# Performance work log

Hardware: AMD Instinct MI355X
Metric: run time of the kernel (lower is better)

## Reference

```python
import jax, jax.numpy as jnp
import numpy as np

N_NODES = 100000
N_EDGES = 800000
D_IN, D_H1, D_H2, D_OUT = 512, 256, 256, 64


def setup_inputs() -> dict:
    key = jax.random.key(0)
    ks = jax.random.split(key, 8)
    x = jax.random.normal(ks[0], (N_NODES, D_IN), dtype=jnp.float32)
    edge_index = jax.random.randint(ks[1], (2, N_EDGES), 0, N_NODES, dtype=jnp.int64)
    # Glorot-style scaled weights (PyG GCNConv uses glorot init; Linear uses kaiming-uniform).
    W1 = jax.random.normal(ks[2], (D_IN, D_H1), dtype=jnp.float32) / np.sqrt(D_IN)
    b1 = jnp.zeros((D_H1,), dtype=jnp.float32)
    W2 = jax.random.normal(ks[3], (D_H1, D_H2), dtype=jnp.float32) / np.sqrt(D_H1)
    b2 = jnp.zeros((D_H2,), dtype=jnp.float32)
    Wc = jax.random.normal(ks[4], (D_H2, D_OUT), dtype=jnp.float32) / np.sqrt(D_H2)
    bc = jnp.zeros((D_OUT,), dtype=jnp.float32)
    return {"x": x, "edge_index": edge_index, "W1": W1, "b1": b1,
            "W2": W2, "b2": b2, "Wc": Wc, "bc": bc}


def reference(x, edge_index, W1, b1, W2, b2, Wc, bc):
    # GCNModel.forward in eval mode (dropout is identity when training=False).
    N = x.shape[0]
    src, dst = edge_index[0], edge_index[1]
    # PyG GCNConv: add self-loops, symmetric normalization D^-1/2 (A+I) D^-1/2.
    deg = jnp.zeros((N,), x.dtype).at[dst].add(jnp.float32(1.0)) + 1.0  # in-degree + self-loop
    dinv = jax.lax.rsqrt(deg)                         # [N]
    norm = dinv[src] * dinv[dst]                      # [E] per-edge coefficient
    self_norm = (dinv * dinv)[:, None]                # [N,1] self-loop coefficient 1/deg

    def gcn_conv(h, W, b):
        h = h @ W                                     # transform first (PyG order)
        agg = jax.ops.segment_sum(h[src] * norm[:, None], dst, num_segments=N)
        return agg + h * self_norm + b

    h = jax.nn.relu(gcn_conv(x, W1, b1))
    h = jax.nn.relu(gcn_conv(h, W2, b2))
    return h @ Wc + bc                                # [N, num_classes]
```

## Files before the change

### kernel.cpp

```cpp
#include <hip/hip_runtime.h>
#include <cstdint>

#define DIN 512
#define DH  256
#define DOUT 64

typedef __attribute__((ext_vector_type(8))) short bf16x8;
typedef __attribute__((ext_vector_type(4))) float f32x4;
typedef unsigned int uint32;

__device__ __forceinline__ unsigned short f2bf(float f) {
    uint32 u = __float_as_uint(f);
    u += 0x7fff + ((u >> 16) & 1);
    return (unsigned short)(u >> 16);
}
__device__ __forceinline__ float bf2f(unsigned short h) {
    return __uint_as_float(((uint32)h) << 16);
}
__device__ __forceinline__ float bflo(uint32 u) { return __uint_as_float(u << 16); }
__device__ __forceinline__ float bfhi(uint32 u) { return __uint_as_float(u & 0xffff0000u); }
__device__ __forceinline__ uint32 pk2(float lo, float hi) {
    return (uint32)f2bf(lo) | ((uint32)f2bf(hi) << 16);
}

__global__ void detect_i64(const unsigned long long* ei, int n_check,
                           unsigned long long bound, int* flag) {
    __shared__ int ok;
    if (threadIdx.x == 0) ok = 1;
    __syncthreads();
    int bad = 0;
    for (int i = threadIdx.x; i < n_check; i += blockDim.x) {
        if (ei[i] >= bound) bad = 1;
    }
    if (bad) ok = 0;
    __syncthreads();
    if (threadIdx.x == 0) *flag = ok;
}

__device__ __forceinline__ int get_idx(const void* ei, int is64, int pos) {
    if (is64) return (int)((const long long*)ei)[pos];
    return ((const int*)ei)[pos];
}

__global__ void count_deg(const void* ei, const int* flag, int E, int* counts) {
    const int is64 = *flag;
    int e = blockIdx.x * blockDim.x + threadIdx.x;
    if (e >= E) return;
    int d = get_idx(ei, is64, E + e);
    atomicAdd(&counts[d], 1);
}

__global__ void compute_dinv(const int* counts, float* dinv, int N) {
    int i = blockIdx.x * blockDim.x + threadIdx.x;
    if (i < N) dinv[i] = rsqrtf((float)counts[i] + 1.0f);
}

#define SCAN_BLOCK 256
#define SCAN_ELEMS 1024

__global__ void scan1(const int* counts, int* out, int* blocksums, int N) {
    __shared__ int sh[SCAN_BLOCK];
    int base = blockIdx.x * SCAN_ELEMS;
    int t = threadIdx.x;
    int v[4];
    int s = 0;
    #pragma unroll
    for (int j = 0; j < 4; j++) {
        int idx = base + t * 4 + j;
        v[j] = (idx < N) ? counts[idx] : 0;
        s += v[j];
    }
    sh[t] = s;
    __syncthreads();
    for (int off = 1; off < SCAN_BLOCK; off <<= 1) {
        int x = (t >= off) ? sh[t - off] : 0;
        __syncthreads();
        sh[t] += x;
        __syncthreads();
    }
    int run = (t == 0) ? 0 : sh[t - 1];
    #pragma unroll
    for (int j = 0; j < 4; j++) {
        int idx = base + t * 4 + j;
        if (idx < N) out[idx] = run;
        run += v[j];
    }
    if (t == SCAN_BLOCK - 1) blocksums[blockIdx.x] = sh[t];
}

__global__ void scan2(int* blocksums, int NB) {
    __shared__ int sh[SCAN_BLOCK];
    int t = threadIdx.x;
    sh[t] = (t < NB) ? blocksums[t] : 0;
    __syncthreads();
    for (int off = 1; off < SCAN_BLOCK; off <<= 1) {
        int x = (t >= off) ? sh[t - off] : 0;
        __syncthreads();
        sh[t] += x;
        __syncthreads();
    }
    if (t < NB) blocksums[t] = (t == 0) ? 0 : sh[t - 1];
}

__global__ void scan3(int* row_ptr, const int* blocksums, int N, int E) {
    int i = blockIdx.x * blockDim.x + threadIdx.x;
    if (i < N) row_ptr[i] += blocksums[i / SCAN_ELEMS];
    if (i == N) row_ptr[N] = E;
}

__global__ void fill_csr(const void* ei, const int* flag, int E,
                         const int* row_ptr, int* cursor, int* col_idx,
                         const float* dinv, float* edge_w) {
    const int is64 = *flag;
    int e = blockIdx.x * blockDim.x + threadIdx.x;
    if (e >= E) return;
    int d = get_idx(ei, is64, E + e);
    int s = get_idx(ei, is64, e);
    int pos = row_ptr[d] + atomicAdd(&cursor[d], 1);
    col_idx[pos] = s;
    edge_w[pos] = dinv[s] * dinv[d];
}

__global__ void transpose_w(const float* __restrict__ W, unsigned short* __restrict__ Bt,
                            int K, int Nw) {
    int i = blockIdx.x * blockDim.x + threadIdx.x;
    if (i >= K * Nw) return;
    int k = i / Nw, n = i % Nw;
    Bt[(size_t)n * K + k] = f2bf(W[i]);
}

template <bool A_FP32>
__global__ __launch_bounds__(256) void gemm_mfma(const void* __restrict__ Ap,
                                                 const unsigned short* __restrict__ Bt,
                                                 unsigned short* __restrict__ C,
                                                 int M, int K) {
    __shared__ unsigned short lds[20480];
    unsigned short* As = lds;
    unsigned short* Bs = lds + 4096;
    const int tid = threadIdx.x;
    const int w = tid >> 6, l = tid & 63;
    const int m0 = blockIdx.x * 64;

    f32x4 acc[4][4] = {};

    for (int k0 = 0; k0 < K; k0 += 64) {
        #pragma unroll
        for (int i = 0; i < 8; i++) {
            int row = i * 32 + (tid >> 3);
            int gq = (tid & 7) ^ (row & 7);
            const unsigned short* src = Bt + (size_t)row * K + k0 + gq * 8;
            unsigned short* dst = Bs + row * 64 + (tid & 7) * 8;
            __builtin_amdgcn_global_load_lds(
                (const __attribute__((address_space(1))) uint32*)src,
                (__attribute__((address_space(3))) uint32*)dst, 16, 0, 0);
        }
        if (A_FP32) {
            const float* Af = (const float*)Ap;
            #pragma unroll
            for (int i = 0; i < 2; i++) {
                int row = i * 32 + (tid >> 3);
                int g = tid & 7;
                int rg = m0 + row; if (rg > M - 1) rg = M - 1;
                const float* s = Af + (size_t)rg * K + k0 + g * 8;
                float4 v0 = *(const float4*)s;
                float4 v1 = *(const float4*)(s + 4);
                uint4 o;
                o.x = pk2(v0.x, v0.y); o.y = pk2(v0.z, v0.w);
                o.z = pk2(v1.x, v1.y); o.w = pk2(v1.z, v1.w);
                *(uint4*)(As + row * 64 + ((g ^ (row & 7)) * 8)) = o;
            }
        } else {
            const unsigned short* Ab = (const unsigned short*)Ap;
            #pragma unroll
            for (int i = 0; i < 2; i++) {
                int row = i * 32 + (tid >> 3);
                int gq = (tid & 7) ^ (row & 7);
                int rg = m0 + row; if (rg > M - 1) rg = M - 1;
                const unsigned short* src = Ab + (size_t)rg * K + k0 + gq * 8;
                unsigned short* dst = As + row * 64 + (tid & 7) * 8;
                __builtin_amdgcn_global_load_lds(
                    (const __attribute__((address_space(1))) uint32*)src,
                    (__attribute__((address_space(3))) uint32*)dst, 16, 0, 0);
            }
        }
        __syncthreads();
        #pragma unroll
        for (int ks = 0; ks < 2; ks++) {
            bf16x8 a[4], b[4];
            #pragma unroll
            for (int m = 0; m < 4; m++) {
                int arow = m * 16 + (l & 15);
                int ag = (ks * 4 + (l >> 4)) ^ (arow & 7);
                a[m] = *(const bf16x8*)(As + arow * 64 + ag * 8);
            }
            #pragma unroll
            for (int n = 0; n < 4; n++) {
                int brow = w * 64 + n * 16 + (l & 15);
                int bg = (ks * 4 + (l >> 4)) ^ (brow & 7);
                b[n] = *(const bf16x8*)(Bs + brow * 64 + bg * 8);
            }
            #pragma unroll
            for (int m = 0; m < 4; m++)
                #pragma unroll
                for (int n = 0; n < 4; n++)
                    acc[m][n] = __builtin_amdgcn_mfma_f32_16x16x32_bf16(a[m], b[n], acc[m][n], 0, 0, 0);
        }
        __syncthreads();
    }

    unsigned short* ep = lds + w * 4096;
    #pragma unroll
    for (int m = 0; m < 4; m++)
        #pragma unroll
        for (int n = 0; n < 4; n++)
            #pragma unroll
            for (int r = 0; r < 4; r++)
                ep[(m * 16 + (l >> 4) * 4 + r) * 64 + n * 16 + (l & 15)] = f2bf(acc[m][n][r]);
    __syncthreads();
    #pragma unroll
    for (int p = 0; p < 8; p++) {
        int row = p * 8 + (l >> 3);
        int gr = m0 + row;
        uint4 v = *(const uint4*)(ep + row * 64 + (l & 7) * 8);
        if (gr < M)
            *(uint4*)(C + (size_t)gr * 256 + w * 64 + (l & 7) * 8) = v;
    }
}

__global__ __launch_bounds__(256) void gemm_head(const unsigned short* __restrict__ A,
                                                 const unsigned short* __restrict__ Bt,
                                                 const float* __restrict__ bias,
                                                 float* __restrict__ out, int M) {
    __shared__ unsigned short As[128 * 64];
    __shared__ unsigned short Bs[64 * 64];
    const int tid = threadIdx.x;
    const int w = tid >> 6, l = tid & 63;
    const int m0 = blockIdx.x * 128;
    const int wr = w >> 1, wc = w & 1;
    f32x4 acc[4][2] = {};

    for (int k0 = 0; k0 < 256; k0 += 64) {
        #pragma unroll
        for (int i = 0; i < 4; i++) {
            int row = i * 32 + (tid >> 3);
            int gq = (tid & 7) ^ (row & 7);
            int rg = m0 + row; if (rg > M - 1) rg = M - 1;
            __builtin_amdgcn_global_load_lds(
                (const __attribute__((address_space(1))) uint32*)(A + (size_t)rg * 256 + k0 + gq * 8),
                (__attribute__((address_space(3))) uint32*)(As + row * 64 + (tid & 7) * 8), 16, 0, 0);
        }
        #pragma unroll
        for (int i = 0; i < 2; i++) {
            int row = i * 32 + (tid >> 3);
            int gq = (tid & 7) ^ (row & 7);
            __builtin_amdgcn_global_load_lds(
                (const __attribute__((address_space(1))) uint32*)(Bt + (size_t)row * 256 + k0 + gq * 8),
                (__attribute__((address_space(3))) uint32*)(Bs + row * 64 + (tid & 7) * 8), 16, 0, 0);
        }
        __syncthreads();
        #pragma unroll
        for (int ks = 0; ks < 2; ks++) {
            bf16x8 a[4], b[2];
            #pragma unroll
            for (int m = 0; m < 4; m++) {
                int arow = wr * 64 + m * 16 + (l & 15);
                int ag = (ks * 4 + (l >> 4)) ^ (arow & 7);
                a[m] = *(const bf16x8*)(As + arow * 64 + ag * 8);
            }
            #pragma unroll
            for (int n = 0; n < 2; n++) {
                int brow = wc * 32 + n * 16 + (l & 15);
                int bg = (ks * 4 + (l >> 4)) ^ (brow & 7);
                b[n] = *(const bf16x8*)(Bs + brow * 64 + bg * 8);
            }
            #pragma unroll
            for (int m = 0; m < 4; m++)
                #pragma unroll
                for (int n = 0; n < 2; n++)
                    acc[m][n] = __builtin_amdgcn_mfma_f32_16x16x32_bf16(a[m], b[n], acc[m][n], 0, 0, 0);
        }
        __syncthreads();
    }
    #pragma unroll
    for (int m = 0; m < 4; m++)
        #pragma unroll
        for (int n = 0; n < 2; n++)
            #pragma unroll
            for (int r = 0; r < 4; r++) {
                int gr = m0 + wr * 64 + m * 16 + (l >> 4) * 4 + r;
                int col = wc * 32 + n * 16 + (l & 15);
                if (gr < M) out[(size_t)gr * 64 + col] = acc[m][n][r] + bias[col];
            }
}

#define ACC8(v, wgt)                                    \
    do {                                                \
        acc[0] = fmaf(wgt, bflo(v.x), acc[0]);          \
        acc[1] = fmaf(wgt, bfhi(v.x), acc[1]);          \
        acc[2] = fmaf(wgt, bflo(v.y), acc[2]);          \
        acc[3] = fmaf(wgt, bfhi(v.y), acc[3]);          \
        acc[4] = fmaf(wgt, bflo(v.z), acc[4]);          \
        acc[5] = fmaf(wgt, bfhi(v.z), acc[5]);          \
        acc[6] = fmaf(wgt, bflo(v.w), acc[6]);          \
        acc[7] = fmaf(wgt, bfhi(v.w), acc[7]);          \
    } while (0)

__global__ __launch_bounds__(256) void aggregate_bf(const unsigned short* __restrict__ t,
                                                    const float* __restrict__ dinv,
                                                    const int* __restrict__ row_ptr,
                                                    const int* __restrict__ col_idx,
                                                    const float* __restrict__ edge_w,
                                                    const float* __restrict__ bias,
                                                    unsigned short* __restrict__ outb,
                                                    int N) {
    int wave = threadIdx.x >> 6;
    int lane = threadIdx.x & 63;
    int half = lane >> 5;
    int sl = lane & 31;
    int n = blockIdx.x * 8 + wave * 2 + half;
    if (n >= N) return;

    float dn = dinv[n];
    int r0 = row_ptr[n], r1 = row_ptr[n + 1];

    float acc[8];
    {
        uint4 sv = *(const uint4*)(t + (size_t)n * DH + sl * 8);
        float sn = dn * dn;
        acc[0] = bflo(sv.x) * sn; acc[1] = bfhi(sv.x) * sn;
        acc[2] = bflo(sv.y) * sn; acc[3] = bfhi(sv.y) * sn;
        acc[4] = bflo(sv.z) * sn; acc[5] = bfhi(sv.z) * sn;
        acc[6] = bflo(sv.w) * sn; acc[7] = bfhi(sv.w) * sn;
    }

    int j = r0;
    for (; j + 4 <= r1; j += 4) {
        int s0 = col_idx[j + 0], s1 = col_idx[j + 1];
        int s2 = col_idx[j + 2], s3 = col_idx[j + 3];
        float w0 = edge_w[j + 0], w1 = edge_w[j + 1];
        float w2 = edge_w[j + 2], w3 = edge_w[j + 3];
        uint4 v0 = *(const uint4*)(t + (size_t)s0 * DH + sl * 8);
        uint4 v1 = *(const uint4*)(t + (size_t)s1 * DH + sl * 8);
        uint4 v2 = *(const uint4*)(t + (size_t)s2 * DH + sl * 8);
        uint4 v3 = *(const uint4*)(t + (size_t)s3 * DH + sl * 8);
        ACC8(v0, w0); ACC8(v1, w1); ACC8(v2, w2); ACC8(v3, w3);
    }
    for (; j < r1; j++) {
        int s = col_idx[j];
        float wgt = edge_w[j];
        uint4 v = *(const uint4*)(t + (size_t)s * DH + sl * 8);
        ACC8(v, wgt);
    }

    float4 b0 = *(const float4*)(bias + sl * 8);
    float4 b1v = *(const float4*)(bias + sl * 8 + 4);
    acc[0] = fmaxf(acc[0] + b0.x, 0.f);  acc[1] = fmaxf(acc[1] + b0.y, 0.f);
    acc[2] = fmaxf(acc[2] + b0.z, 0.f);  acc[3] = fmaxf(acc[3] + b0.w, 0.f);
    acc[4] = fmaxf(acc[4] + b1v.x, 0.f); acc[5] = fmaxf(acc[5] + b1v.y, 0.f);
    acc[6] = fmaxf(acc[6] + b1v.z, 0.f); acc[7] = fmaxf(acc[7] + b1v.w, 0.f);

    uint4 o;
    o.x = pk2(acc[0], acc[1]);
    o.y = pk2(acc[2], acc[3]);
    o.z = pk2(acc[4], acc[5]);
    o.w = pk2(acc[6], acc[7]);
    *(uint4*)(outb + (size_t)n * DH + sl * 8) = o;
}

extern "C" void kernel_launch(void* const* d_in, const int* in_sizes, int n_in,
                              void* d_out, int out_size, void* d_ws, size_t ws_size,
                              hipStream_t stream) {
    const float* x  = (const float*)d_in[0];
    const void*  ei = d_in[1];
    const float* W1 = (const float*)d_in[2];
    const float* b1 = (const float*)d_in[3];
    const float* W2 = (const float*)d_in[4];
    const float* b2 = (const float*)d_in[5];
    const float* Wc = (const float*)d_in[6];
    const float* bc = (const float*)d_in[7];
    float* out = (float*)d_out;

    const int N = in_sizes[0] / DIN;
    const int E = in_sizes[1] / 2;

    char* ws = (char*)d_ws;
    size_t off = 0;
    auto alloc = [&](size_t bytes) -> void* {
        off = (off + 255) & ~(size_t)255;
        void* p = ws + off;
        off += bytes;
        return p;
    };

    int*   flag      = (int*)alloc(4);
    int*   counts    = (int*)alloc((size_t)N * 4);
    int*   row_ptr   = (int*)alloc((size_t)(N + 1) * 4);
    int*   col_idx   = (int*)alloc((size_t)E * 4);
    float* edge_w    = (float*)alloc((size_t)E * 4);
    int*   blocksums = (int*)alloc(1024 * 4);
    float* dinv      = (float*)alloc((size_t)N * 4);
    unsigned short* Bt1   = (unsigned short*)alloc((size_t)DH * DIN * 2);
    unsigned short* Bt2   = (unsigned short*)alloc((size_t)DH * DH * 2);
    unsigned short* Btc   = (unsigned short*)alloc((size_t)DOUT * DH * 2);
    unsigned short* t_buf = (unsigned short*)alloc((size_t)N * DH * 2);
    unsigned short* a_buf = (unsigned short*)alloc((size_t)N * DH * 2);

    const int NB = (N + SCAN_ELEMS - 1) / SCAN_ELEMS;
    const int gM64  = (N + 63) / 64;
    const int gM128 = (N + 127) / 128;

    detect_i64<<<1, 256, 0, stream>>>((const unsigned long long*)ei, 1024,
                                      (unsigned long long)N, flag);
    transpose_w<<<(DIN * DH + 255) / 256, 256, 0, stream>>>(W1, Bt1, DIN, DH);
    transpose_w<<<(DH * DH + 255) / 256, 256, 0, stream>>>(W2, Bt2, DH, DH);
    transpose_w<<<(DH * DOUT + 255) / 256, 256, 0, stream>>>(Wc, Btc, DH, DOUT);

    hipMemsetAsync(counts, 0, (size_t)N * 4, stream);
    count_deg<<<(E + 255) / 256, 256, 0, stream>>>(ei, flag, E, counts);
    compute_dinv<<<(N + 255) / 256, 256, 0, stream>>>(counts, dinv, N);
    scan1<<<NB, SCAN_BLOCK, 0, stream>>>(counts, row_ptr, blocksums, N);
    scan2<<<1, SCAN_BLOCK, 0, stream>>>(blocksums, NB);
    scan3<<<(N + 1 + 255) / 256, 256, 0, stream>>>(row_ptr, blocksums, N, E);
    hipMemsetAsync(counts, 0, (size_t)N * 4, stream);
    fill_csr<<<(E + 255) / 256, 256, 0, stream>>>(ei, flag, E, row_ptr, counts, col_idx,
                                                  dinv, edge_w);

    gemm_mfma<true><<<gM64, 256, 0, stream>>>(x, Bt1, t_buf, N, DIN);
    aggregate_bf<<<(N + 7) / 8, 256, 0, stream>>>(t_buf, dinv, row_ptr, col_idx, edge_w, b1, a_buf, N);
    gemm_mfma<false><<<gM64, 256, 0, stream>>>(a_buf, Bt2, t_buf, N, DH);
    aggregate_bf<<<(N + 7) / 8, 256, 0, stream>>>(t_buf, dinv, row_ptr, col_idx, edge_w, b2, a_buf, N);
    gemm_head<<<gM128, 256, 0, stream>>>(a_buf, Btc, bc, out, N);
}
```

Measured before the change: 364.0 us.

## Fuse neighbor aggregation into following GEMMs and read B fragments from global

Merges each aggregation pass with the next GEMM. A block aggregates 64 rows into LDS as swizzled bf16 and then runs the MFMA GEMM on that tile directly, which removes the intermediate a_buf round trip through HBM and two kernel launches. B fragments in all GEMMs are now loaded straight from global memory (small weights, expected to be cache resident) instead of staged through LDS. The trade-offs are serialized aggregation inside each GEMM block, with fewer rows per wave in flight, and possibly higher-latency B loads in the MFMA loop.

```diff
diff --git a/kernel.cpp b/kernel.cpp
--- a/kernel.cpp
+++ b/kernel.cpp
@@ -13,9 +13,6 @@
     uint32 u = __float_as_uint(f);
     u += 0x7fff + ((u >> 16) & 1);
     return (unsigned short)(u >> 16);
-}
-__device__ __forceinline__ float bf2f(unsigned short h) {
-    return __uint_as_float(((uint32)h) << 16);
 }
 __device__ __forceinline__ float bflo(uint32 u) { return __uint_as_float(u << 16); }
 __device__ __forceinline__ float bfhi(uint32 u) { return __uint_as_float(u & 0xffff0000u); }
@@ -129,14 +126,12 @@
     Bt[(size_t)n * K + k] = f2bf(W[i]);
 }
 
-template <bool A_FP32>
-__global__ __launch_bounds__(256) void gemm_mfma(const void* __restrict__ Ap,
-                                                 const unsigned short* __restrict__ Bt,
-                                                 unsigned short* __restrict__ C,
-                                                 int M, int K) {
-    __shared__ unsigned short lds[20480];
+__global__ __launch_bounds__(256) void gemm1_mfma(const float* __restrict__ Af,
+                                                  const unsigned short* __restrict__ Bt,
+                                                  unsigned short* __restrict__ C,
+                                                  int M, int K) {
+    __shared__ unsigned short lds[16384];
     unsigned short* As = lds;
-    unsigned short* Bs = lds + 4096;
     const int tid = threadIdx.x;
     const int w = tid >> 6, l = tid & 63;
     const int m0 = blockIdx.x * 64;
@@ -144,44 +139,19 @@
     f32x4 acc[4][4] = {};
 
     for (int k0 = 0; k0 < K; k0 += 64) {
-        #pragma unroll
-        for (int i = 0; i < 8; i++) {
+        __syncthreads();
+        #pragma unroll
+        for (int i = 0; i < 2; i++) {
             int row = i * 32 + (tid >> 3);
-            int gq = (tid & 7) ^ (row & 7);
-            const unsigned short* src = Bt + (size_t)row * K + k0 + gq * 8;
-            unsigned short* dst = Bs + row * 64 + (tid & 7) * 8;
-            __builtin_amdgcn_global_load_lds(
-                (const __attribute__((address_space(1))) uint32*)src,
-                (__attribute__((address_space(3))) uint32*)dst, 16, 0, 0);
-        }
-        if (A_FP32) {
-            const float* Af = (const float*)Ap;
-            #pragma unroll
-            for (int i = 0; i < 2; i++) {
-                int row = i * 32 + (tid >> 3);
-                int g = tid & 7;
-                int rg = m0 + row; if (rg > M - 1) rg = M - 1;
-                const float* s = Af + (size_t)rg * K + k0 + g * 8;
-                float4 v0 = *(const float4*)s;
-                float4 v1 = *(const float4*)(s + 4);
-                uint4 o;
-                o.x = pk2(v0.x, v0.y); o.y = pk2(v0.z, v0.w);
-                o.z = pk2(v1.x, v1.y); o.w = pk2(v1.z, v1.w);
-                *(uint4*)(As + row * 64 + ((g ^ (row & 7)) * 8)) = o;
-            }
-        } else {
-            const unsigned short* Ab = (const unsigned short*)Ap;
-            #pragma unroll
-            for (int i = 0; i < 2; i++) {
-                int row = i * 32 + (tid >> 3);
-                int gq = (tid & 7) ^ (row & 7);
-                int rg = m0 + row; if (rg > M - 1) rg = M - 1;
-                const unsigned short* src = Ab + (size_t)rg * K + k0 + gq * 8;
-                unsigned short* dst = As + row * 64 + (tid & 7) * 8;
-                __builtin_amdgcn_global_load_lds(
-                    (const __attribute__((address_space(1))) uint32*)src,
-                    (__attribute__((address_space(3))) uint32*)dst, 16, 0, 0);
-            }
+            int g = tid & 7;
+            int rg = m0 + row; if (rg > M - 1) rg = M - 1;
+            const float* s = Af + (size_t)rg * K + k0 + g * 8;
+            float4 v0 = *(const float4*)s;
+            float4 v1 = *(const float4*)(s + 4);
+            uint4 o;
+            o.x = pk2(v0.x, v0.y); o.y = pk2(v0.z, v0.w);
+            o.z = pk2(v1.x, v1.y); o.w = pk2(v1.z, v1.w);
+            *(uint4*)(As + row * 64 + ((g ^ (row & 7)) * 8)) = o;
         }
         __syncthreads();
         #pragma unroll
@@ -189,15 +159,14 @@
             bf16x8 a[4], b[4];
             #pragma unroll
             for (int m = 0; m < 4; m++) {
-                int arow = m * 16 + (l & 15);
-                int ag = (ks * 4 + (l >> 4)) ^ (arow & 7);
-                a[m] = *(const bf16x8*)(As + arow * 64 + ag * 8);
+                int ar = m * 16 + (l & 15);
+                int q = (ks * 4 + (l >> 4)) ^ (ar & 7);
+                a[m] = *(const bf16x8*)(As + ar * 64 + q * 8);
             }
             #pragma unroll
             for (int n = 0; n < 4; n++) {
-                int brow = w * 64 + n * 16 + (l & 15);
-                int bg = (ks * 4 + (l >> 4)) ^ (brow & 7);
-                b[n] = *(const bf16x8*)(Bs + brow * 64 + bg * 8);
+                int br = w * 64 + n * 16 + (l & 15);
+                b[n] = *(const bf16x8*)(Bt + (size_t)br * K + k0 + ks * 32 + (l >> 4) * 8);
             }
             #pragma unroll
             for (int m = 0; m < 4; m++)
@@ -205,9 +174,8 @@
                 for (int n = 0; n < 4; n++)
                     acc[m][n] = __builtin_amdgcn_mfma_f32_16x16x32_bf16(a[m], b[n], acc[m][n], 0, 0, 0);
         }
-        __syncthreads();
-    }
-
+    }
+    __syncthreads();
     unsigned short* ep = lds + w * 4096;
     #pragma unroll
     for (int m = 0; m < 4; m++)
@@ -225,72 +193,6 @@
         if (gr < M)
             *(uint4*)(C + (size_t)gr * 256 + w * 64 + (l & 7) * 8) = v;
     }
-}
-
-__global__ __launch_bounds__(256) void gemm_head(const unsigned short* __restrict__ A,
-                                                 const unsigned short* __restrict__ Bt,
-                                                 const float* __restrict__ bias,
-                                                 float* __restrict__ out, int M) {
-    __shared__ unsigned short As[128 * 64];
-    __shared__ unsigned short Bs[64 * 64];
-    const int tid = threadIdx.x;
-    const int w = tid >> 6, l = tid & 63;
-    const int m0 = blockIdx.x * 128;
-    const int wr = w >> 1, wc = w & 1;
-    f32x4 acc[4][2] = {};
-
-    for (int k0 = 0; k0 < 256; k0 += 64) {
-        #pragma unroll
-        for (int i = 0; i < 4; i++) {
-            int row = i * 32 + (tid >> 3);
-            int gq = (tid & 7) ^ (row & 7);
-            int rg = m0 + row; if (rg > M - 1) rg = M - 1;
-            __builtin_amdgcn_global_load_lds(
-                (const __attribute__((address_space(1))) uint32*)(A + (size_t)rg * 256 + k0 + gq * 8),
-                (__attribute__((address_space(3))) uint32*)(As + row * 64 + (tid & 7) * 8), 16, 0, 0);
-        }
-        #pragma unroll
-        for (int i = 0; i < 2; i++) {
-            int row = i * 32 + (tid >> 3);
-            int gq = (tid & 7) ^ (row & 7);
-            __builtin_amdgcn_global_load_lds(
-                (const __attribute__((address_space(1))) uint32*)(Bt + (size_t)row * 256 + k0 + gq * 8),
-                (__attribute__((address_space(3))) uint32*)(Bs + row * 64 + (tid & 7) * 8), 16, 0, 0);
-        }
-        __syncthreads();
-        #pragma unroll
-        for (int ks = 0; ks < 2; ks++) {
-            bf16x8 a[4], b[2];
-            #pragma unroll
-            for (int m = 0; m < 4; m++) {
-                int arow = wr * 64 + m * 16 + (l & 15);
-                int ag = (ks * 4 + (l >> 4)) ^ (arow & 7);
-                a[m] = *(const bf16x8*)(As + arow * 64 + ag * 8);
-            }
-            #pragma unroll
-            for (int n = 0; n < 2; n++) {
-                int brow = wc * 32 + n * 16 + (l & 15);
-                int bg = (ks * 4 + (l >> 4)) ^ (brow & 7);
-                b[n] = *(const bf16x8*)(Bs + brow * 64 + bg * 8);
-            }
-            #pragma unroll
-            for (int m = 0; m < 4; m++)
-                #pragma unroll
-                for (int n = 0; n < 2; n++)
-                    acc[m][n] = __builtin_amdgcn_mfma_f32_16x16x32_bf16(a[m], b[n], acc[m][n], 0, 0, 0);
-        }
-        __syncthreads();
-    }
-    #pragma unroll
-    for (int m = 0; m < 4; m++)
-        #pragma unroll
-        for (int n = 0; n < 2; n++)
-            #pragma unroll
-            for (int r = 0; r < 4; r++) {
-                int gr = m0 + wr * 64 + m * 16 + (l >> 4) * 4 + r;
-                int col = wc * 32 + n * 16 + (l & 15);
-                if (gr < M) out[(size_t)gr * 64 + col] = acc[m][n][r] + bias[col];
-            }
 }
 
 #define ACC8(v, wgt)                                    \
@@ -305,24 +207,15 @@
         acc[7] = fmaf(wgt, bfhi(v.w), acc[7]);          \
     } while (0)
 
-__global__ __launch_bounds__(256) void aggregate_bf(const unsigned short* __restrict__ t,
-                                                    const float* __restrict__ dinv,
-                                                    const int* __restrict__ row_ptr,
-                                                    const int* __restrict__ col_idx,
-                                                    const float* __restrict__ edge_w,
-                                                    const float* __restrict__ bias,
-                                                    unsigned short* __restrict__ outb,
-                                                    int N) {
-    int wave = threadIdx.x >> 6;
-    int lane = threadIdx.x & 63;
-    int half = lane >> 5;
-    int sl = lane & 31;
-    int n = blockIdx.x * 8 + wave * 2 + half;
-    if (n >= N) return;
-
+__device__ __forceinline__ uint4 agg_row(const unsigned short* __restrict__ t,
+                                         const float* __restrict__ dinv,
+                                         const int* __restrict__ row_ptr,
+                                         const int* __restrict__ col_idx,
+                                         const float* __restrict__ edge_w,
+                                         const float* __restrict__ bias,
+                                         int n, int sl) {
     float dn = dinv[n];
     int r0 = row_ptr[n], r1 = row_ptr[n + 1];
-
     float acc[8];
     {
         uint4 sv = *(const uint4*)(t + (size_t)n * DH + sl * 8);
@@ -332,7 +225,6 @@
         acc[4] = bflo(sv.z) * sn; acc[5] = bfhi(sv.z) * sn;
         acc[6] = bflo(sv.w) * sn; acc[7] = bfhi(sv.w) * sn;
     }
-
     int j = r0;
     for (; j + 4 <= r1; j += 4) {
         int s0 = col_idx[j + 0], s1 = col_idx[j + 1];
@@ -351,20 +243,143 @@
         uint4 v = *(const uint4*)(t + (size_t)s * DH + sl * 8);
         ACC8(v, wgt);
     }
-
     float4 b0 = *(const float4*)(bias + sl * 8);
     float4 b1v = *(const float4*)(bias + sl * 8 + 4);
     acc[0] = fmaxf(acc[0] + b0.x, 0.f);  acc[1] = fmaxf(acc[1] + b0.y, 0.f);
     acc[2] = fmaxf(acc[2] + b0.z, 0.f);  acc[3] = fmaxf(acc[3] + b0.w, 0.f);
     acc[4] = fmaxf(acc[4] + b1v.x, 0.f); acc[5] = fmaxf(acc[5] + b1v.y, 0.f);
     acc[6] = fmaxf(acc[6] + b1v.z, 0.f); acc[7] = fmaxf(acc[7] + b1v.w, 0.f);
-
     uint4 o;
     o.x = pk2(acc[0], acc[1]);
     o.y = pk2(acc[2], acc[3]);
     o.z = pk2(acc[4], acc[5]);
     o.w = pk2(acc[6], acc[7]);
-    *(uint4*)(outb + (size_t)n * DH + sl * 8) = o;
+    return o;
+}
+
+__global__ __launch_bounds__(256) void fused_mid(const unsigned short* __restrict__ t,
+                                                 const float* __restrict__ dinv,
+                                                 const int* __restrict__ row_ptr,
+                                                 const int* __restrict__ col_idx,
+                                                 const float* __restrict__ edge_w,
+                                                 const float* __restrict__ bias,
+                                                 const unsigned short* __restrict__ Bt,
+                                                 unsigned short* __restrict__ C,
+                                                 int N) {
+    __shared__ unsigned short As[16384];
+    const int tid = threadIdx.x;
+    const int w = tid >> 6, l = tid & 63;
+    const int half = l >> 5, sl = l & 31;
+    const int m0 = blockIdx.x * 64;
+
+    #pragma unroll 1
+    for (int i = 0; i < 8; i++) {
+        int row = i * 8 + w * 2 + half;
+        int n = m0 + row;
+        uint4 o = make_uint4(0, 0, 0, 0);
+        if (n < N) o = agg_row(t, dinv, row_ptr, col_idx, edge_w, bias, n, sl);
+        *(uint4*)(As + row * 256 + ((sl ^ (row & 7)) * 8)) = o;
+    }
+    __syncthreads();
+
+    f32x4 acc[4][4] = {};
+    #pragma unroll
+    for (int kt = 0; kt < 4; kt++) {
+        #pragma unroll
+        for (int ks = 0; ks < 2; ks++) {
+            bf16x8 a[4], b[4];
+            #pragma unroll
+            for (int m = 0; m < 4; m++) {
+                int ar = m * 16 + (l & 15);
+                int q = (kt * 8 + ks * 4 + (l >> 4)) ^ (ar & 7);
+                a[m] = *(const bf16x8*)(As + ar * 256 + q * 8);
+            }
+            #pragma unroll
+            for (int n = 0; n < 4; n++) {
+                int br = w * 64 + n * 16 + (l & 15);
+                b[n] = *(const bf16x8*)(Bt + (size_t)br * 256 + kt * 64 + ks * 32 + (l >> 4) * 8);
+            }
+            #pragma unroll
+            for (int m = 0; m < 4; m++)
+                #pragma unroll
+                for (int n = 0; n < 4; n++)
+                    acc[m][n] = __builtin_amdgcn_mfma_f32_16x16x32_bf16(a[m], b[n], acc[m][n], 0, 0, 0);
+        }
+    }
+    __syncthreads();
+
+    unsigned short* ep = As + w * 4096;
+    #pragma unroll
+    for (int m = 0; m < 4; m++)
+        #pragma unroll
+        for (int n = 0; n < 4; n++)
+            #pragma unroll
+            for (int r = 0; r < 4; r++)
+                ep[(m * 16 + (l >> 4) * 4 + r) * 64 + n * 16 + (l & 15)] = f2bf(acc[m][n][r]);
+    __syncthreads();
+    #pragma unroll
+    for (int p = 0; p < 8; p++) {
+        int row = p * 8 + (l >> 3);
+        int gr = m0 + row;
+        uint4 v = *(const uint4*)(ep + row * 64 + (l & 7) * 8);
+        if (gr < N)
+            *(uint4*)(C + (size_t)gr * 256 + w * 64 + (l & 7) * 8) = v;
+    }
+}
+
+__global__ __launch_bounds__(256) void fused_head(const unsigned short* __restrict__ t2,
+                                                  const float* __restrict__ dinv,
+                                                  const int* __restrict__ row_ptr,
+                                                  const int* __restrict__ col_idx,
+                                                  const float* __restrict__ edge_w,
+                                                  const float* __restrict__ b2,
+                                                  const unsigned short* __restrict__ Btc,
+                                                  const float* __restrict__ bc,
+                                                  float* __restrict__ out,
+                                                  int N) {
+    __shared__ unsigned short As[16384];
+    const int tid = threadIdx.x;
+    const int w = tid >> 6, l = tid & 63;
+    const int half = l >> 5, sl = l & 31;
+    const int m0 = blockIdx.x * 64;
+
+    #pragma unroll 1
+    for (int i = 0; i < 8; i++) {
+        int row = i * 8 + w * 2 + half;
+        int n = m0 + row;
+        uint4 o = make_uint4(0, 0, 0, 0);
+        if (n < N) o = agg_row(t2, dinv, row_ptr, col_idx, edge_w, b2, n, sl);
+        *(uint4*)(As + row * 256 + ((sl ^ (row & 7)) * 8)) = o;
+    }
+    __syncthreads();
+
+    f32x4 acc[4] = {};
+    #pragma unroll
+    for (int kt = 0; kt < 4; kt++) {
+        #pragma unroll
+        for (int ks = 0; ks < 2; ks++) {
+            int ar = w * 16 + (l & 15);
+            int q = (kt * 8 + ks * 4 + (l >> 4)) ^ (ar & 7);
+            bf16x8 a = *(const bf16x8*)(As + ar * 256 + q * 8);
+            bf16x8 b[4];
+            #pragma unroll
+            for (int n = 0; n < 4; n++) {
+                int br = n * 16 + (l & 15);
+                b[n] = *(const bf16x8*)(Btc + (size_t)br * 256 + kt * 64 + ks * 32 + (l >> 4) * 8);
+            }
+            #pragma unroll
+            for (int n = 0; n < 4; n++)
+                acc[n] = __builtin_amdgcn_mfma_f32_16x16x32_bf16(a, b[n], acc[n], 0, 0, 0);
+        }
+    }
+    #pragma unroll
+    for (int n = 0; n < 4; n++)
+        #pragma unroll
+        for (int r = 0; r < 4; r++) {
+            int gr = m0 + w * 16 + (l >> 4) * 4 + r;
+            int col = n * 16 + (l & 15);
+            if (gr < N) out[(size_t)gr * 64 + col] = acc[n][r] + bc[col];
+        }
 }
 
 extern "C" void kernel_launch(void* const* d_in, const int* in_sizes, int n_in,
@@ -403,11 +418,10 @@
     unsigned short* Bt2   = (unsigned short*)alloc((size_t)DH * DH * 2);
     unsigned short* Btc   = (unsigned short*)alloc((size_t)DOUT * DH * 2);
     unsigned short* t_buf = (unsigned short*)alloc((size_t)N * DH * 2);
-    unsigned short* a_buf = (unsigned short*)alloc((size_t)N * DH * 2);
+    unsigned short* t2    = (unsigned short*)alloc((size_t)N * DH * 2);
 
     const int NB = (N + SCAN_ELEMS - 1) / SCAN_ELEMS;
-    const int gM64  = (N + 63) / 64;
-    const int gM128 = (N + 127) / 128;
+    const int gM64 = (N + 63) / 64;
 
     detect_i64<<<1, 256, 0, stream>>>((const unsigned long long*)ei, 1024,
                                       (unsigned long long)N, flag);
@@ -425,9 +439,7 @@
     fill_csr<<<(E + 255) / 256, 256, 0, stream>>>(ei, flag, E, row_ptr, counts, col_idx,
                                                   dinv, edge_w);
 
-    gemm_mfma<true><<<gM64, 256, 0, stream>>>(x, Bt1, t_buf, N, DIN);
-    aggregate_bf<<<(N + 7) / 8, 256, 0, stream>>>(t_buf, dinv, row_ptr, col_idx, edge_w, b1, a_buf, N);
-    gemm_mfma<false><<<gM64, 256, 0, stream>>>(a_buf, Bt2, t_buf, N, DH);
-    aggregate_bf<<<(N + 7) / 8, 256, 0, stream>>>(t_buf, dinv, row_ptr, col_idx, edge_w, b2, a_buf, N);
-    gemm_head<<<gM128, 256, 0, stream>>>(a_buf, Btc, bc, out, N);
-}
+    gemm1_mfma<<<gM64, 256, 0, stream>>>(x, Bt1, t_buf, N, DIN);
+    fused_mid<<<gM64, 256, 0, stream>>>(t_buf, dinv, row_ptr, col_idx, edge_w, b1, Bt2, t2, N);
+    fused_head<<<gM64, 256, 0, stream>>>(t2, dinv, row_ptr, col_idx, edge_w, b2, Btc, bc, out, N);
+}
```

New measurement: 447.7 us. 1.23x slower.

## Double-buffer A tiles in LDS and read B fragments directly from global

Applied to the files above, without the earlier changes.

Restructures the GEMM main loop to prefetch the next A tile (fp32 into registers, or bf16 via global_load_lds into the alternate buffer) while MFMAs run on the current one, using two LDS buffers and one barrier per iteration. The B (weight) tile is no longer staged in LDS; each wave loads its bf16x8 fragments straight from global memory, relying on cache since the weights are small and shared. This aims to hide global load latency and cut LDS traffic and size. The risk is higher-latency uncoalesced global loads for B inside the compute loop, which could stall the MFMAs.

```diff
diff --git a/kernel.cpp b/kernel.cpp
--- a/kernel.cpp
+++ b/kernel.cpp
@@ -13,9 +13,6 @@
     uint32 u = __float_as_uint(f);
     u += 0x7fff + ((u >> 16) & 1);
     return (unsigned short)(u >> 16);
-}
-__device__ __forceinline__ float bf2f(unsigned short h) {
-    return __uint_as_float(((uint32)h) << 16);
 }
 __device__ __forceinline__ float bflo(uint32 u) { return __uint_as_float(u << 16); }
 __device__ __forceinline__ float bfhi(uint32 u) { return __uint_as_float(u & 0xffff0000u); }
@@ -134,76 +131,103 @@
                                                  const unsigned short* __restrict__ Bt,
                                                  unsigned short* __restrict__ C,
                                                  int M, int K) {
-    __shared__ unsigned short lds[20480];
-    unsigned short* As = lds;
-    unsigned short* Bs = lds + 4096;
+    __shared__ unsigned short lds[16384];
     const int tid = threadIdx.x;
     const int w = tid >> 6, l = tid & 63;
     const int m0 = blockIdx.x * 64;
+    const int nk = K >> 6;
+
+    const float* Af = (const float*)Ap;
+    const unsigned short* Ab = (const unsigned short*)Ap;
 
     f32x4 acc[4][4] = {};
-
-    for (int k0 = 0; k0 < K; k0 += 64) {
-        #pragma unroll
-        for (int i = 0; i < 8; i++) {
-            int row = i * 32 + (tid >> 3);
-            int gq = (tid & 7) ^ (row & 7);
-            const unsigned short* src = Bt + (size_t)row * K + k0 + gq * 8;
-            unsigned short* dst = Bs + row * 64 + (tid & 7) * 8;
+    float4 ra0, ra1, ra2, ra3;
+
+    const int srow0 = (tid >> 3);
+    const int sg = tid & 7;
+    int rg0 = m0 + srow0;      if (rg0 > M - 1) rg0 = M - 1;
+    int rg1 = m0 + srow0 + 32; if (rg1 > M - 1) rg1 = M - 1;
+
+    if (A_FP32) {
+        const float* s0 = Af + (size_t)rg0 * K + sg * 8;
+        const float* s1 = Af + (size_t)rg1 * K + sg * 8;
+        ra0 = *(const float4*)s0; ra1 = *(const float4*)(s0 + 4);
+        ra2 = *(const float4*)s1; ra3 = *(const float4*)(s1 + 4);
+        uint4 o0, o1;
+        o0.x = pk2(ra0.x, ra0.y); o0.y = pk2(ra0.z, ra0.w);
+        o0.z = pk2(ra1.x, ra1.y); o0.w = pk2(ra1.z, ra1.w);
+        o1.x = pk2(ra2.x, ra2.y); o1.y = pk2(ra2.z, ra2.w);
+        o1.z = pk2(ra3.x, ra3.y); o1.w = pk2(ra3.z, ra3.w);
+        *(uint4*)(lds + srow0 * 64 + ((sg ^ (srow0 & 7)) * 8)) = o0;
+        *(uint4*)(lds + (srow0 + 32) * 64 + ((sg ^ ((srow0 + 32) & 7)) * 8)) = o1;
+    } else {
+        #pragma unroll
+        for (int i = 0; i < 2; i++) {
+            int row = i * 32 + srow0;
+            int gq = sg ^ (row & 7);
+            int rg = (i == 0) ? rg0 : rg1;
             __builtin_amdgcn_global_load_lds(
-                (const __attribute__((address_space(1))) uint32*)src,
-                (__attribute__((address_space(3))) uint32*)dst, 16, 0, 0);
-        }
-        if (A_FP32) {
-            const float* Af = (const float*)Ap;
-            #pragma unroll
-            for (int i = 0; i < 2; i++) {
-                int row = i * 32 + (tid >> 3);
-                int g = tid & 7;
-                int rg = m0 + row; if (rg > M - 1) rg = M - 1;
-                const float* s = Af + (size_t)rg * K + k0 + g * 8;
-                float4 v0 = *(const float4*)s;
-                float4 v1 = *(const float4*)(s + 4);
-                uint4 o;
-                o.x = pk2(v0.x, v0.y); o.y = pk2(v0.z, v0.w);
-                o.z = pk2(v1.x, v1.y); o.w = pk2(v1.z, v1.w);
-                *(uint4*)(As + row * 64 + ((g ^ (row & 7)) * 8)) = o;
-            }
-        } else {
-            const unsigned short* Ab = (const unsigned short*)Ap;
-            #pragma unroll
-            for (int i = 0; i < 2; i++) {
-                int row = i * 32 + (tid >> 3);
-                int gq = (tid & 7) ^ (row & 7);
-                int rg = m0 + row; if (rg > M - 1) rg = M - 1;
-                const unsigned short* src = Ab + (size_t)rg * K + k0 + gq * 8;
-                unsigned short* dst = As + row * 64 + (tid & 7) * 8;
-                __builtin_amdgcn_global_load_lds(
-                    (const __attribute__((address_space(1))) uint32*)src,
-                    (__attribute__((address_space(3))) uint32*)dst, 16, 0, 0);
-            }
-        }
-        __syncthreads();
+                (const __attribute__((address_space(1))) uint32*)(Ab + (size_t)rg * K + gq * 8),
+                (__attribute__((address_space(3))) uint32*)(lds + row * 64 + sg * 8), 16, 0, 0);
+        }
+    }
+    __syncthreads();
+
+    for (int k = 0; k < nk; k++) {
+        unsigned short* cur = lds + (k & 1) * 4096;
+        unsigned short* nxt = lds + ((k + 1) & 1) * 4096;
+        const int k0 = k << 6;
+        const bool more = (k + 1 < nk);
+
+        if (more) {
+            const int k0n = k0 + 64;
+            if (A_FP32) {
+                const float* s0 = Af + (size_t)rg0 * K + k0n + sg * 8;
+                const float* s1 = Af + (size_t)rg1 * K + k0n + sg * 8;
+                ra0 = *(const float4*)s0; ra1 = *(const float4*)(s0 + 4);
+                ra2 = *(const float4*)s1; ra3 = *(const float4*)(s1 + 4);
+            } else {
+                #pragma unroll
+                for (int i = 0; i < 2; i++) {
+                    int row = i * 32 + srow0;
+                    int gq = sg ^ (row & 7);
+                    int rg = (i == 0) ? rg0 : rg1;
+                    __builtin_amdgcn_global_load_lds(
+                        (const __attribute__((address_space(1))) uint32*)(Ab + (size_t)rg * K + k0n + gq * 8),
+                        (__attribute__((address_space(3))) uint32*)(nxt + row * 64 + sg * 8), 16, 0, 0);
+                }
+            }
+        }
+
         #pragma unroll
         for (int ks = 0; ks < 2; ks++) {
             bf16x8 a[4], b[4];
             #pragma unroll
             for (int m = 0; m < 4; m++) {
-                int arow = m * 16 + (l & 15);
-                int ag = (ks * 4 + (l >> 4)) ^ (arow & 7);
-                a[m] = *(const bf16x8*)(As + arow * 64 + ag * 8);
+                int ar = m * 16 + (l & 15);
+                int q = (ks * 4 + (l >> 4)) ^ (ar & 7);
+                a[m] = *(const bf16x8*)(cur + ar * 64 + q * 8);
             }
             #pragma unroll
             for (int n = 0; n < 4; n++) {
-                int brow = w * 64 + n * 16 + (l & 15);
-                int bg = (ks * 4 + (l >> 4)) ^ (brow & 7);
-                b[n] = *(const bf16x8*)(Bs + brow * 64 + bg * 8);
+                int br = w * 64 + n * 16 + (l & 15);
+                b[n] = *(const bf16x8*)(Bt + (size_t)br * K + k0 + ks * 32 + (l >> 4) * 8);
             }
             #pragma unroll
             for (int m = 0; m < 4; m++)
                 #pragma unroll
                 for (int n = 0; n < 4; n++)
                     acc[m][n] = __builtin_amdgcn_mfma_f32_16x16x32_bf16(a[m], b[n], acc[m][n], 0, 0, 0);
+        }
+
+        if (A_FP32 && more) {
+            uint4 o0, o1;
+            o0.x = pk2(ra0.x, ra0.y); o0.y = pk2(ra0.z, ra0.w);
+            o0.z = pk2(ra1.x, ra1.y); o0.w = pk2(ra1.z, ra1.w);
+            o1.x = pk2(ra2.x, ra2.y); o1.y = pk2(ra2.z, ra2.w);
+            o1.z = pk2(ra3.x, ra3.y); o1.w = pk2(ra3.z, ra3.w);
+            *(uint4*)(nxt + srow0 * 64 + ((sg ^ (srow0 & 7)) * 8)) = o0;
+            *(uint4*)(nxt + (srow0 + 32) * 64 + ((sg ^ ((srow0 + 32) & 7)) * 8)) = o1;
         }
         __syncthreads();
     }
```

After: 387.3 us. 6.4% more time.

## Use persistent GEMM kernel with LDS-resident W2 for second layer

Applied to the files above, without the earlier changes.

Replaces the generic tiled MFMA GEMM for layer 2 with a persistent kernel of 256 blocks of 512 threads. Each block loads the whole transposed W2 (256x256 bf16, 128KB) into LDS once, then loops over 64-row tiles of A, double-buffering A chunks with direct global-to-LDS loads. The aim is to avoid reloading B tiles for every output tile. In exchange it needs a very large LDS footprint that limits occupancy to one block per CU, and it stores the output with scalar 2-byte writes.

```diff
diff --git a/kernel.cpp b/kernel.cpp
--- a/kernel.cpp
+++ b/kernel.cpp
@@ -13,9 +13,6 @@
     uint32 u = __float_as_uint(f);
     u += 0x7fff + ((u >> 16) & 1);
     return (unsigned short)(u >> 16);
-}
-__device__ __forceinline__ float bf2f(unsigned short h) {
-    return __uint_as_float(((uint32)h) << 16);
 }
 __device__ __forceinline__ float bflo(uint32 u) { return __uint_as_float(u << 16); }
 __device__ __forceinline__ float bfhi(uint32 u) { return __uint_as_float(u & 0xffff0000u); }
@@ -224,6 +221,92 @@
         uint4 v = *(const uint4*)(ep + row * 64 + (l & 7) * 8);
         if (gr < M)
             *(uint4*)(C + (size_t)gr * 256 + w * 64 + (l & 7) * 8) = v;
+    }
+}
+
+__global__ __launch_bounds__(512) void gemm2_persist(const unsigned short* __restrict__ A,
+                                                     const unsigned short* __restrict__ Bt,
+                                                     unsigned short* __restrict__ C,
+                                                     int M) {
+    __shared__ unsigned short lds[73728];
+    unsigned short* Bs = lds;
+    unsigned short* As = lds + 65536;
+    const int tid = threadIdx.x;
+    const int w = tid >> 6, l = tid & 63;
+    const int wr = w >> 2, wc = w & 3;
+
+    #pragma unroll
+    for (int i = 0; i < 16; i++) {
+        int gi = i * 512 + tid;
+        int r = gi >> 5, g = gi & 31;
+        int gs = g ^ (r & 7);
+        __builtin_amdgcn_global_load_lds(
+            (const __attribute__((address_space(1))) uint32*)(Bt + (size_t)r * 256 + gs * 8),
+            (__attribute__((address_space(3))) uint32*)(Bs + (size_t)gi * 8), 16, 0, 0);
+    }
+
+    const int sr = tid >> 3;
+    const int sg = tid & 7;
+
+    for (int mt = blockIdx.x; mt * 64 < M; mt += gridDim.x) {
+        const int m0 = mt * 64;
+        {
+            int rg = m0 + sr; if (rg > M - 1) rg = M - 1;
+            int gq = sg ^ (sr & 7);
+            __builtin_amdgcn_global_load_lds(
+                (const __attribute__((address_space(1))) uint32*)(A + (size_t)rg * 256 + gq * 8),
+                (__attribute__((address_space(3))) uint32*)(As + tid * 8), 16, 0, 0);
+        }
+        __syncthreads();
+
+        f32x4 acc[2][4] = {};
+        #pragma unroll
+        for (int k = 0; k < 4; k++) {
+            if (k < 3) {
+                int rg = m0 + sr; if (rg > M - 1) rg = M - 1;
+                int gq = sg ^ (sr & 7);
+                __builtin_amdgcn_global_load_lds(
+                    (const __attribute__((address_space(1))) uint32*)(A + (size_t)rg * 256 + (k + 1) * 64 + gq * 8),
+                    (__attribute__((address_space(3))) uint32*)(As + ((k + 1) & 1) * 4096 + tid * 8), 16, 0, 0);
+            }
+            const unsigned short* Ab = As + (k & 1) * 4096;
+            #pragma unroll
+            for (int ks = 0; ks < 2; ks++) {
+                bf16x8 a[2], b[4];
+                #pragma unroll
+                for (int m = 0; m < 2; m++) {
+                    int ar = wr * 32 + m * 16 + (l & 15);
+                    int q = (ks * 4 + (l >> 4)) ^ (ar & 7);
+                    a[m] = *(const bf16x8*)(Ab + ar * 64 + q * 8);
+                }
+                #pragma unroll
+                for (int n = 0; n < 4; n++) {
+                    int br = wc * 64 + n * 16 + (l & 15);
+                    int gabs = k * 8 + ks * 4 + (l >> 4);
+                    int q = gabs ^ (br & 7);
+                    b[n] = *(const bf16x8*)(Bs + br * 256 + q * 8);
+                }
+                #pragma unroll
+                for (int m = 0; m < 2; m++)
+                    #pragma unroll
+                    for (int n = 0; n < 4; n++)
+                        acc[m][n] = __builtin_amdgcn_mfma_f32_16x16x32_bf16(a[m], b[n], acc[m][n], 0, 0, 0);
+            }
+            __syncthreads();
+        }
+
+        #pragma unroll
+        for (int m = 0; m < 2; m++)
+            #pragma unroll
+            for (int r = 0; r < 4; r++) {
+                int row = m0 + wr * 32 + m * 16 + (l >> 4) * 4 + r;
+                if (row >= M) continue;
+                #pragma unroll
+                for (int n = 0; n < 4; n++) {
+                    int col = wc * 64 + n * 16 + (l & 15);
+                    C[(size_t)row * 256 + col] = f2bf(acc[m][n][r]);
+                }
+            }
     }
 }
 
@@ -427,7 +510,7 @@
 
     gemm_mfma<true><<<gM64, 256, 0, stream>>>(x, Bt1, t_buf, N, DIN);
     aggregate_bf<<<(N + 7) / 8, 256, 0, stream>>>(t_buf, dinv, row_ptr, col_idx, edge_w, b1, a_buf, N);
-    gemm_mfma<false><<<gM64, 256, 0, stream>>>(a_buf, Bt2, t_buf, N, DH);
+    gemm2_persist<<<256, 512, 0, stream>>>(a_buf, Bt2, t_buf, N);
     aggregate_bf<<<(N + 7) / 8, 256, 0, stream>>>(t_buf, dinv, row_ptr, col_idx, edge_w, b2, a_buf, N);
     gemm_head<<<gM128, 256, 0, stream>>>(a_buf, Btc, bc, out, N);
 }
```

Result: faster. 356.6 us (-2.0%).
